# Kernel tuning notes

Hardware: AMD Instinct MI355X
Metric: run time of the kernel (lower is better)

The kernel has to match this reference:

```python
import jax, jax.numpy as jnp
import numpy as np

QC = 13        # quantum_channel
NQ = 12        # qubits per patch circuit
LAYERS12 = 3   # num_layer for FQConv ansatz
LAYERS4 = 4    # layers for the 4-qubit basic ansatz
GROUPS = 10
DIM = 40       # 3*QC + 1 channels
B = 1024
TDIM = 128
EPS = 1e-6     # flax GroupNorm default epsilon
TWO_PI = 2.0 * float(np.pi)


def _take2(s, ax):
    return jnp.take(s, 0, axis=ax), jnp.take(s, 1, axis=ax)


def init_state(n, N):
    # |0...0> state, shape (N, 2, 2, ..., 2); wire w lives on axis w+1
    s = jnp.zeros((N, 2 ** n), jnp.complex64).at[:, 0].set(1.0)
    return s.reshape((N,) + (2,) * n)


def apply_rx(state, theta, w):
    # RX(theta) = [[c, -i s], [-i s, c]], c=cos(theta/2), s=sin(theta/2)
    ax = w + 1
    theta = jnp.asarray(theta, jnp.float32)
    c = jnp.cos(0.5 * theta)
    s = jnp.sin(0.5 * theta)
    if theta.ndim > 0:  # per-sample angles (data embedding)
        sh = (-1,) + (1,) * (state.ndim - 2)
        c = c.reshape(sh)
        s = s.reshape(sh)
    c = c.astype(state.dtype)
    js = (1j * s).astype(state.dtype)
    s0, s1 = _take2(state, ax)
    return jnp.stack([c * s0 - js * s1, c * s1 - js * s0], axis=ax)


def apply_cnot(state, c, t):
    ca = c + 1
    ta = t + 1 if t < c else t  # target axis inside the control=1 slice
    s0, s1 = _take2(state, ca)
    return jnp.stack([s0, jnp.flip(s1, axis=ta)], axis=ca)


def apply_crz(state, theta, c, t):
    # CRZ = diag(1, 1, e^{-i theta/2}, e^{+i theta/2})
    ca = c + 1
    ta = t + 1 if t < c else t
    s0, s1 = _take2(state, ca)
    t0, t1 = _take2(s1, ta)
    em = jnp.exp(-0.5j * theta).astype(state.dtype)
    ep = jnp.exp(0.5j * theta).astype(state.dtype)
    s1 = jnp.stack([em * t0, ep * t1], axis=ta)
    return jnp.stack([s0, s1], axis=ca)


def apply_crx(state, theta, c, t):
    # controlled RX on target when control = 1
    ca = c + 1
    ta = t + 1 if t < c else t
    s0, s1 = _take2(state, ca)
    t0, t1 = _take2(s1, ta)
    ch = jnp.cos(0.5 * theta).astype(state.dtype)
    js = (1j * jnp.sin(0.5 * theta)).astype(state.dtype)
    s1 = jnp.stack([ch * t0 - js * t1, ch * t1 - js * t0], axis=ta)
    return jnp.stack([s0, s1], axis=ca)


def expvals_z(state, n):
    # <Z_w> = P(bit_w = 0) - P(bit_w = 1)
    p = jnp.real(state * jnp.conj(state))
    zs = []
    for w in range(n):
        axes = tuple(a for a in range(1, n + 1) if a != w + 1)
        q = p.sum(axis=axes)  # (N, 2)
        zs.append(q[:, 0] - q[:, 1])
    return jnp.stack(zs, axis=-1)  # (N, n)


def fqconv_layer(state, th):
    # zip(range(11,-1,-4), range(12)) -> i in (11,7,3), j in (0,1,2)
    for j, i in enumerate((11, 7, 3)):
        w1 = [i - 3, i - 2, i - 1, i] + [(i + k) % NQ for k in (1, 2, 3, 4)]
        tj = th[8 * j: 8 * (j + 1)]
        for bi, bj in zip(range(3, -1, -1), range(4)):  # block_C: CRZ
            state = apply_crz(state, TWO_PI * tj[bj], w1[bi + 4], w1[bi])
        for bi, bj in zip(range(3, -1, -1), range(4)):  # block_D: CRX
            state = apply_crx(state, TWO_PI * tj[4 + bj], w1[bi + 4], w1[bi])
    return state


def circuit12(x, theta):
    # x: (N, 12) angles; theta: (72,)
    state = init_state(NQ, x.shape[0])
    for w in range(NQ):  # AngleEmbedding, rotation='X'
        state = apply_rx(state, x[:, w], w)
    for l in range(LAYERS12):
        state = fqconv_layer(state, theta[24 * l: 24 * (l + 1)])
    return expvals_z(state, NQ)


def circuit4(x, theta):
    # Basic_ansatz, 4 qubits, 4 layers, 4 params/layer
    state = init_state(4, x.shape[0])
    for w in range(4):
        state = apply_rx(state, x[:, w], w)
    for l in range(LAYERS4):
        for w in range(4):
            state = apply_rx(state, theta[4 * l + w], w)
        for w in range(3):
            state = apply_cnot(state, w, w + 1)
        state = apply_cnot(state, 3, 0)
    return expvals_z(state, 4)


def run12_all(y, params, circ):
    # scan over the QC per-channel circuits (same structure, different params)
    def body(carry, xp):
        yy, th = xp
        return carry, circ(yy, th)
    _, zs = jax.lax.scan(body, None, (y, params))
    return zs  # (QC, N, 12)


def group_norm(h, scale, bias):
    Bn, H, W, C = h.shape
    g = h.reshape(Bn, H, W, GROUPS, C // GROUPS)
    mu = g.mean(axis=(1, 2, 4), keepdims=True)
    var = g.var(axis=(1, 2, 4), keepdims=True)
    g = (g - mu) * jax.lax.rsqrt(var + EPS)
    return g.reshape(Bn, H, W, C) * scale + bias


def forward(x, time_emb, qparams12, qparams4, gn0_scale, gn0_bias,
            gn1_scale, gn1_bias, time_w, time_b, circ12=circuit12):
    Bn = x.shape[0]

    def qpass(inp, p12_block):
        # per-channel 12-qubit circuits on 2x2x3 patches
        y = jnp.stack([inp[..., 3 * i:3 * (i + 1)].reshape(-1, 12) for i in range(QC)], 0)
        z = run12_all(y, p12_block, circ12)                      # (QC, Bn, 12)
        h1 = jnp.moveaxis(z.reshape(QC, Bn, 2, 2, 3), 0, -2).reshape(Bn, 2, 2, 3 * QC)
        # NOTE: faithful to the source, BOTH passes use circuit/params[-2]
        h4 = circuit4(inp[..., 3 * QC:].reshape(-1, 4), qparams4[0]).reshape(Bn, 2, 2, 1)
        return jnp.concatenate([h1, h4], axis=-1)                 # (Bn, 2, 2, 40)

    h = qpass(x, qparams12[:QC])
    h = group_norm(h, gn0_scale, gn0_bias)
    t = jax.nn.swish(time_emb) @ time_w + time_b                  # (Bn, 2*DIM)
    scale, shift = jnp.split(t[:, None, None, :], 2, axis=-1)
    h = jax.nn.swish(h * (1.0 + scale) + shift)
    h = qpass(h, qparams12[QC:])
    h = jax.nn.swish(group_norm(h, gn1_scale, gn1_bias))
    return x + h  # C == dim, so no res_conv


def setup_inputs() -> dict:
    key = jax.random.key(0)
    ks = jax.random.split(key, 5)
    return {
        "x": jax.random.normal(ks[0], (B, 2, 2, DIM), jnp.float32),
        "time_emb": jax.random.normal(ks[1], (B, TDIM), jnp.float32),
        "qparams12": jax.random.uniform(ks[2], (2 * QC, 24 * LAYERS12), jnp.float32),
        "qparams4": jax.random.uniform(ks[3], (2, 16), jnp.float32),
        "gn0_scale": jnp.ones((DIM,), jnp.float32),
        "gn0_bias": jnp.zeros((DIM,), jnp.float32),
        "gn1_scale": jnp.ones((DIM,), jnp.float32),
        "gn1_bias": jnp.zeros((DIM,), jnp.float32),
        "time_w": jax.random.normal(ks[4], (TDIM, 2 * DIM), jnp.float32) * (TDIM ** -0.5),
        "time_b": jnp.zeros((2 * DIM,), jnp.float32),
    }


def reference(x, time_emb, qparams12, qparams4, gn0_scale, gn0_bias,
              gn1_scale, gn1_bias, time_w, time_b):
    return forward(x, time_emb, qparams12, qparams4, gn0_scale, gn0_bias,
                   gn1_scale, gn1_bias, time_w, time_b)
```

## Files before the change

kernel.cpp:

```cpp
#include <hip/hip_runtime.h>
#include <math.h>


#define PI_F 3.14159265358979323846f

#define DPP_XOR1 0xB1
#define DPP_XOR2 0x4E
#define DPP_XOR8 0x128

typedef float f2 __attribute__((ext_vector_type(2)));

template<int CTRL>
__device__ __forceinline__ float dppf(float x)
{
    return __int_as_float(__builtin_amdgcn_update_dpp(
        __float_as_int(x), __float_as_int(x), CTRL, 0xF, 0xF, false));
}

template<int CTRL>
__device__ __forceinline__ f2 dpp2v(f2 v)
{
    f2 r;
    r[0] = dppf<CTRL>(v[0]);
    r[1] = dppf<CTRL>(v[1]);
    return r;
}

__device__ __forceinline__ float swz4f(float x)
{
    return __int_as_float(__builtin_amdgcn_ds_swizzle(__float_as_int(x), 0x101F));
}

__device__ __forceinline__ f2 swz4v(f2 v)
{
    f2 r;
    r[0] = swz4f(v[0]);
    r[1] = swz4f(v[1]);
    return r;
}

__device__ __forceinline__ float swz16f(float x)
{
    return __int_as_float(__builtin_amdgcn_ds_swizzle(__float_as_int(x), 0x401F));
}

__device__ __forceinline__ f2 swz16v(f2 v)
{
    f2 r;
    r[0] = swz16f(v[0]);
    r[1] = swz16f(v[1]);
    return r;
}

__device__ __forceinline__ float psum16(float x)
{
    float c, d;
    asm("v_mov_b32 %0, %2\n\t"
        "v_mov_b32 %1, %2\n\t"
        "v_permlane16_swap_b32 %0, %1"
        : "=&v"(c), "=&v"(d)
        : "v"(x));
    return c + d;
}

__device__ __forceinline__ float psum32(float x)
{
    float c, d;
    asm("v_mov_b32 %0, %2\n\t"
        "v_mov_b32 %1, %2\n\t"
        "v_permlane32_swap_b32 %0, %1"
        : "=&v"(c), "=&v"(d)
        : "v"(x));
    return c + d;
}

__device__ __forceinline__ void crz_g0_fused(const float* a, f2* R, f2* I,
                                             int lane, int wq)
{
    float gr[4], gi[4];
#pragma unroll
    for (int m = 0; m < 4; ++m) {
        bool cb;
        if      (m == 0) cb = (lane >> 4) & 1;
        else if (m == 1) cb = (lane >> 5) & 1;
        else if (m == 2) cb = wq & 1;
        else             cb = (wq >> 1) & 1;
        gr[m] = cb ? a[2 * m]     : 1.0f;
        gi[m] = cb ? a[2 * m + 1] : 0.0f;
    }
    float u0 = gr[1] * gr[0], v0 = gi[1] * gi[0];
    float w0 = gr[1] * gi[0], z0 = gi[1] * gr[0];
    float p01r[2] = { u0 - v0, u0 + v0 };
    float p01i[2] = { -(w0 + z0), w0 - z0 };
    float u1 = gr[3] * gr[2], v1 = gi[3] * gi[2];
    float w1 = gr[3] * gi[2], z1 = gi[3] * gr[2];
    float p23r[2] = { u1 - v1, u1 + v1 };
    float p23i[2] = { -(w1 + z1), w1 - z1 };

    f2 MrV[4], MiV[4];
#pragma unroll
    for (int p = 0; p < 4; ++p) {
#pragma unroll
        for (int e = 0; e < 2; ++e) {
            const int t = 2 * p + e;
            const int t10 = t & 3, t2 = (t >> 2) & 1;
            float br = (t10 == 0 || t10 == 3) ? p01r[0] : p01r[1];
            float bi = (t10 == 0) ? p01i[0] : (t10 == 1) ? p01i[1]
                     : (t10 == 2) ? -p01i[1] : -p01i[0];
            MrV[p][e] = p23r[t2] * br - p23i[t2] * bi;
            MiV[p][e] = p23r[t2] * bi + p23i[t2] * br;
        }
    }
#pragma unroll
    for (int j = 0; j < 4; ++j) {
        f2 mr = MrV[j], mi = MiV[j];
        f2 r = R[j], im = I[j];
        R[j] = mr * r - mi * im;
        I[j] = mr * im + mi * r;
    }
#pragma unroll
    for (int j = 4; j < 8; ++j) {
        f2 mr = __builtin_shufflevector(MrV[7 - j], MrV[7 - j], 1, 0);
        f2 mi = __builtin_shufflevector(MiV[7 - j], MiV[7 - j], 1, 0);
        f2 r = R[j], im = I[j];
        R[j] = mr * r + mi * im;
        I[j] = mr * im - mi * r;
    }
}

__device__ __forceinline__ void crx_pair(float cg, float sg, f2* R, f2* I)
{
#pragma unroll
    for (int j = 0; j < 8; ++j) {
        f2 r = R[j], im = I[j];
        f2 rs = __builtin_shufflevector(r, r, 1, 0);
        f2 is = __builtin_shufflevector(im, im, 1, 0);
        R[j] = cg * r + sg * is;
        I[j] = cg * im - sg * rs;
    }
}

template<int M>
__device__ __forceinline__ void crx_elem(float cg, float sg, f2* R, f2* I)
{
#pragma unroll
    for (int j = 0; j < 8; ++j) {
        if (j & M) continue;
        const int p = j | M;
        f2 r0 = R[j], i0 = I[j], r1 = R[p], i1 = I[p];
        R[j] = cg * r0 + sg * i1;  I[j] = cg * i0 - sg * r1;
        R[p] = cg * r1 + sg * i0;  I[p] = cg * i1 - sg * r0;
    }
}

__device__ __forceinline__ void crz_e(float cg, float ss, f2* R, f2* I)
{
    const f2 mrv = {1.0f, cg};
    const f2 miv = {0.0f, ss};
#pragma unroll
    for (int j = 0; j < 8; ++j) {
        f2 r = R[j], im = I[j];
        R[j] = mrv * r - miv * im;
        I[j] = mrv * im + miv * r;
    }
}

template<int CB>
__device__ __forceinline__ void crz_ctrlj(float cg, float ss, f2* R, f2* I)
{
#pragma unroll
    for (int j = 0; j < 8; ++j) {
        if (!((j >> CB) & 1)) continue;
        f2 r = R[j], im = I[j];
        R[j] = cg * r - ss * im;
        I[j] = cg * im + ss * r;
    }
}

__device__ __forceinline__ void crx_sh_e(float cg, float sg, f2* R, f2* I)
{
    const f2 cgv = {1.0f, cg};
    const f2 sgv = {0.0f, sg};
#pragma unroll
    for (int j = 0; j < 8; ++j) {
        f2 br = dpp2v<DPP_XOR1>(R[j]);
        f2 bi = dpp2v<DPP_XOR1>(I[j]);
        f2 r = R[j], im = I[j];
        R[j] = cgv * r + sgv * bi;
        I[j] = cgv * im - sgv * br;
    }
}

template<int CB, int CTRL>
__device__ __forceinline__ void crx_shj_dpp(float cg, float sg, f2* R, f2* I)
{
#pragma unroll
    for (int j = 0; j < 8; ++j) {
        if (!((j >> CB) & 1)) continue;
        f2 br = dpp2v<CTRL>(R[j]);
        f2 bi = dpp2v<CTRL>(I[j]);
        f2 r = R[j], im = I[j];
        R[j] = cg * r + sg * bi;
        I[j] = cg * im - sg * br;
    }
}

template<int CB>
__device__ __forceinline__ void crx_shj_swz4(float cg, float sg, f2* R, f2* I)
{
#pragma unroll
    for (int j = 0; j < 8; ++j) {
        if (!((j >> CB) & 1)) continue;
        f2 br = swz4v(R[j]);
        f2 bi = swz4v(I[j]);
        f2 r = R[j], im = I[j];
        R[j] = cg * r + sg * bi;
        I[j] = cg * im - sg * br;
    }
}

__device__ __forceinline__ void crz_g2_fused(const float* a, f2* R, f2* I,
                                             int lane, int wq)
{
    float s0 = ((lane >> 4) & 1) ? a[1] : -a[1];
    bool  c0 = lane & 1;
    float f0r = c0 ? a[0] : 1.0f, f0i = c0 ? s0 : 0.0f;
    float s1 = ((lane >> 5) & 1) ? a[3] : -a[3];
    bool  c1 = (lane >> 1) & 1;
    float f1r = c1 ? a[2] : 1.0f, f1i = c1 ? s1 : 0.0f;
    float s2 = (wq & 1) ? a[5] : -a[5];
    bool  c2 = (lane >> 2) & 1;
    float f2r = c2 ? a[4] : 1.0f, f2i = c2 ? s2 : 0.0f;
    float s3 = ((wq >> 1) & 1) ? a[7] : -a[7];
    bool  c3 = (lane >> 3) & 1;
    float f3r = c3 ? a[6] : 1.0f, f3i = c3 ? s3 : 0.0f;
    float t01r = f0r * f1r - f0i * f1i, t01i = f0r * f1i + f0i * f1r;
    float t23r = f2r * f3r - f2i * f3i, t23i = f2r * f3i + f2i * f3r;
    float Pr = t01r * t23r - t01i * t23i;
    float Pi = t01r * t23i + t01i * t23r;
#pragma unroll
    for (int j = 0; j < 8; ++j) {
        f2 r = R[j], im = I[j];
        R[j] = Pr * r - Pi * im;
        I[j] = Pr * im + Pi * r;
    }
}

__device__ __forceinline__ void crx_swz16_all(float cg, float sg, f2* R, f2* I)
{
#pragma unroll
    for (int j = 0; j < 8; ++j) {
        f2 br = swz16v(R[j]);
        f2 bi = swz16v(I[j]);
        f2 r = R[j], im = I[j];
        R[j] = cg * r + sg * bi;
        I[j] = cg * im - sg * br;
    }
}

__device__ __forceinline__ void crx_perm32(float cg, float sg, f2* R, f2* I)
{
#pragma unroll
    for (int j = 0; j < 8; ++j) {
        float a0 = R[j][0], b0 = I[j][0];
        float a1 = R[j][1], b1 = I[j][1];
        asm("v_permlane32_swap_b32 %0, %1\n\t"
            "v_permlane32_swap_b32 %1, %0" : "+v"(a0), "+v"(b0));
        asm("v_permlane32_swap_b32 %0, %1\n\t"
            "v_permlane32_swap_b32 %1, %0" : "+v"(a1), "+v"(b1));
        f2 A = {a0, a1}, Bv = {b0, b1};
        f2 r = R[j], im = I[j];
        R[j] = cg * r + sg * A;
        I[j] = cg * im - sg * Bv;
    }
}

__global__ void __launch_bounds__(256, 4)
qpass12_kernel(const float* __restrict__ inp, const float* __restrict__ cs,
               float* __restrict__ outp)
{
    __shared__ f2 xbufv[4 * 32 * 17];
    float* xbuff = reinterpret_cast<float*>(xbufv);
    const int ts   = threadIdx.x;
    const int wq   = ts >> 6;
    const int lane = ts & 63;
    const int sim  = blockIdx.x;
    const int ci = sim % 13;
    const int b  = sim / 13;
    const float* csc = cs + ci * 144;
    const int ibase = b * 160 + ci * 3;

    float cw[12], sw[12];
#pragma unroll
    for (int w = 0; w < 12; ++w) {
        float x = inp[ibase + (w / 3) * 40 + (w % 3)];
        __sincosf(0.5f * x, &sw[w], &cw[w]);
    }

    float pref = ((wq >> 1) ? sw[0] : cw[0]) * ((wq & 1) ? sw[1] : cw[1]);
#pragma unroll
    for (int w = 2; w < 8; ++w)
        pref *= ((lane >> (7 - w)) & 1) ? sw[w] : cw[w];

    const int pl = (__popc(lane) + __popc(wq)) & 3;
    float oa = (pl == 0) ? 1.0f : (pl == 2) ? -1.0f : 0.0f;
    float ob = (pl == 1) ? -1.0f : (pl == 3) ? 1.0f : 0.0f;

    f2 R[8], I[8];
#pragma unroll
    for (int j = 0; j < 8; ++j) {
        float base = pref * ((j & 4) ? sw[8] : cw[8]) *
                     ((j & 2) ? sw[9] : cw[9]) * ((j & 1) ? sw[10] : cw[10]);
        f2 v2 = { base * cw[11], base * sw[11] };
        const int q0 = __popc(j) & 3;
        const int q1 = (q0 + 1) & 3;
        const float c0l = (q0 == 0) ? oa : (q0 == 1) ? ob : (q0 == 2) ? -oa : -ob;
        const float c1l = (q0 == 0) ? ob : (q0 == 1) ? -oa : (q0 == 2) ? -ob : oa;
        const float c0h = (q1 == 0) ? oa : (q1 == 1) ? ob : (q1 == 2) ? -oa : -ob;
        const float c1h = (q1 == 0) ? ob : (q1 == 1) ? -oa : (q1 == 2) ? -ob : oa;
        R[j] = f2{ v2[0] * c0l, v2[1] * c0h };
        I[j] = f2{ v2[0] * c1l, v2[1] * c1h };
    }

    const bool act2 = (lane >> 2) & 1;
    const bool act3 = (lane >> 3) & 1;
    const int ai2 = ((lane >> 3) << 2) | (lane & 3);
    const int ai3 = ((lane >> 4) << 3) | (lane & 7);
    f2* xw2 = &xbufv[(wq * 32 + ai2) * 17];
    f2* xr2 = &xbufv[((wq ^ 1) * 32 + ai2) * 17];
    f2* xw3 = &xbufv[(wq * 32 + ai3) * 17];
    f2* xr3 = &xbufv[((wq ^ 2) * 32 + ai3) * 17];

#pragma unroll 1
    for (int l = 0; l < 3; ++l) {
        const float* a = csc + l * 48;

        crz_g0_fused(a, R, I, lane, wq);
        { bool cb = (lane >> 4) & 1;
          crx_pair(cb ? a[ 8] : 1.0f, cb ? a[ 9] : 0.0f, R, I); }
        { bool cb = (lane >> 5) & 1;
          crx_elem<1>(cb ? a[10] : 1.0f, cb ? a[11] : 0.0f, R, I); }
        if (wq & 1)
            crx_elem<2>(a[12], a[13], R, I);
        if ((wq >> 1) & 1)
            crx_elem<4>(a[14], a[15], R, I);

        { float ss = (lane & 1) ? a[17] : -a[17];
          crz_e(a[16], ss, R, I); }
        { float ss = ((lane >> 1) & 1) ? a[19] : -a[19];
          crz_ctrlj<0>(a[18], ss, R, I); }
        { float ss = ((lane >> 2) & 1) ? a[21] : -a[21];
          crz_ctrlj<1>(a[20], ss, R, I); }
        { float ss = ((lane >> 3) & 1) ? a[23] : -a[23];
          crz_ctrlj<2>(a[22], ss, R, I); }
        crx_sh_e(a[24], a[25], R, I);
        crx_shj_dpp<0, DPP_XOR2>(a[26], a[27], R, I);
        crx_shj_swz4<1>(a[28], a[29], R, I);
        crx_shj_dpp<2, DPP_XOR8>(a[30], a[31], R, I);

        crz_g2_fused(a + 32, R, I, lane, wq);
        { bool cb = lane & 1;
          crx_swz16_all(cb ? a[40] : 1.0f, cb ? a[41] : 0.0f, R, I); }
        { bool cb = (lane >> 1) & 1;
          crx_perm32(cb ? a[42] : 1.0f, cb ? a[43] : 0.0f, R, I); }
        __syncthreads();
        if (act2) {
#pragma unroll
            for (int j = 0; j < 8; ++j) {
                xw2[j]     = R[j];
                xw2[8 + j] = I[j];
            }
        }
        __syncthreads();
        if (act2) {
            float cg = a[44], sg = a[45];
#pragma unroll
            for (int j = 0; j < 8; ++j) {
                f2 br = xr2[j], bi = xr2[8 + j];
                f2 r = R[j], im = I[j];
                R[j] = cg * r + sg * bi;
                I[j] = cg * im - sg * br;
            }
        }
        __syncthreads();
        if (act3) {
#pragma unroll
            for (int j = 0; j < 8; ++j) {
                xw3[j]     = R[j];
                xw3[8 + j] = I[j];
            }
        }
        __syncthreads();
        if (act3) {
            float cg = a[46], sg = a[47];
#pragma unroll
            for (int j = 0; j < 8; ++j) {
                f2 br = xr3[j], bi = xr3[8 + j];
                f2 r = R[j], im = I[j];
                R[j] = cg * r + sg * bi;
                I[j] = cg * im - sg * br;
            }
        }
    }

    f2 accT = {0.0f, 0.0f}, acc8 = {0.0f, 0.0f};
    f2 acc9 = {0.0f, 0.0f}, acc10 = {0.0f, 0.0f};
#pragma unroll
    for (int j = 0; j < 8; ++j) {
        f2 p = R[j] * R[j] + I[j] * I[j];
        accT += p;
        if (j & 4) acc8 -= p; else acc8 += p;
        if (j & 2) acc9 -= p; else acc9 += p;
        if (j & 1) acc10 -= p; else acc10 += p;
    }
    float T   = accT[0] + accT[1];
    float A11 = accT[0] - accT[1];
    float A8  = acc8[0] + acc8[1];
    float A9  = acc9[0] + acc9[1];
    float A10 = acc10[0] + acc10[1];

    float dc0, dc1, dc2, dc3, dc4, dc5;
    float x = T;
    { float u = dppf<DPP_XOR1>(x); dc0 = x - u; x += u; }
    { float u = dppf<DPP_XOR2>(x); dc1 = x - u; x += u; }
    { float u = swz4f(x);          dc2 = x - u; x += u; }
    { float u = dppf<DPP_XOR8>(x); dc3 = x - u; x += u; }
    { float s = psum16(x);         dc4 = 2.0f * x - s; x = s; }
    { float s = psum32(x);         dc5 = 2.0f * x - s; x = s; }
    dc0 += dppf<DPP_XOR2>(dc0);
    dc0 += swz4f(dc0);
    dc0 += dppf<DPP_XOR8>(dc0);
    dc0 = psum16(dc0);  dc0 = psum32(dc0);
    dc1 += swz4f(dc1);
    dc1 += dppf<DPP_XOR8>(dc1);
    dc1 = psum16(dc1);  dc1 = psum32(dc1);
    dc2 += dppf<DPP_XOR8>(dc2);
    dc2 = psum16(dc2);  dc2 = psum32(dc2);
    dc3 = psum16(dc3);  dc3 = psum32(dc3);
    dc4 = psum32(dc4);
    A8  += dppf<DPP_XOR1>(A8);   A8  += dppf<DPP_XOR2>(A8);
    A8  += swz4f(A8);            A8  += dppf<DPP_XOR8>(A8);
    A8  = psum16(A8);            A8  = psum32(A8);
    A9  += dppf<DPP_XOR1>(A9);   A9  += dppf<DPP_XOR2>(A9);
    A9  += swz4f(A9);            A9  += dppf<DPP_XOR8>(A9);
    A9  = psum16(A9);            A9  = psum32(A9);
    A10 += dppf<DPP_XOR1>(A10);  A10 += dppf<DPP_XOR2>(A10);
    A10 += swz4f(A10);           A10 += dppf<DPP_XOR8>(A10);
    A10 = psum16(A10);           A10 = psum32(A10);
    A11 += dppf<DPP_XOR1>(A11);  A11 += dppf<DPP_XOR2>(A11);
    A11 += swz4f(A11);           A11 += dppf<DPP_XOR8>(A11);
    A11 = psum16(A11);           A11 = psum32(A11);

    __syncthreads();
    if (lane == 0) {
        float* wv = &xbuff[wq * 12];
        wv[0]  = (wq >> 1) ? -x : x;
        wv[1]  = (wq & 1)  ? -x : x;
        wv[2]  = dc5;
        wv[3]  = dc4;
        wv[4]  = dc3;
        wv[5]  = dc2;
        wv[6]  = dc1;
        wv[7]  = dc0;
        wv[8]  = A8;
        wv[9]  = A9;
        wv[10] = A10;
        wv[11] = A11;
    }
    __syncthreads();
    if (ts < 12) {
        float z = xbuff[ts] + xbuff[12 + ts] + xbuff[24 + ts] + xbuff[36 + ts];
        outp[ibase + (ts / 3) * 40 + (ts % 3)] = z;
    }
}

__global__ void q4_kernel(const float* __restrict__ inp,
                          const float* __restrict__ cs4,
                          float* __restrict__ outp)
{
    int b = blockIdx.x * blockDim.x + threadIdx.x;
    if (b >= 1024) return;
    float cw[4], sw[4];
#pragma unroll
    for (int j = 0; j < 4; ++j) {
        float x = inp[(b * 4 + j) * 40 + 39];
        __sincosf(0.5f * x, &sw[j], &cw[j]);
    }
    float sr[16], si[16];
#pragma unroll
    for (int k = 0; k < 16; ++k) {
        float v = 1.0f;
#pragma unroll
        for (int j = 0; j < 4; ++j)
            v *= ((k >> (3 - j)) & 1) ? sw[j] : cw[j];
        int ph = __popc(k) & 3;
        sr[k] = (ph == 0) ? v : (ph == 2) ? -v : 0.0f;
        si[k] = (ph == 1) ? -v : (ph == 3) ? v : 0.0f;
    }
#pragma unroll
    for (int l = 0; l < 4; ++l) {
#pragma unroll
        for (int w = 0; w < 4; ++w) {
            float cg = cs4[2 * (4 * l + w)], sg = cs4[2 * (4 * l + w) + 1];
            const int m = 1 << (3 - w);
#pragma unroll
            for (int k = 0; k < 16; ++k) {
                if (k & m) continue;
                int p2 = k | m;
                float r0 = sr[k], i0 = si[k], r1 = sr[p2], i1 = si[p2];
                sr[k]  = cg * r0 + sg * i1;  si[k]  = cg * i0 - sg * r1;
                sr[p2] = cg * r1 + sg * i0;  si[p2] = cg * i1 - sg * r0;
            }
        }
#pragma unroll
        for (int e = 0; e < 4; ++e) {
            const int cq = e, tq = (e + 1) & 3;
            const int pcb = 1 << (3 - cq), ptb = 1 << (3 - tq);
#pragma unroll
            for (int k = 0; k < 16; ++k) {
                if (!(k & pcb)) continue;
                if (k & ptb) continue;
                int p2 = k | ptb;
                float tr = sr[k], ti = si[k];
                sr[k] = sr[p2]; si[k] = si[p2];
                sr[p2] = tr;    si[p2] = ti;
            }
        }
    }
    float p[16];
#pragma unroll
    for (int k = 0; k < 16; ++k) p[k] = sr[k] * sr[k] + si[k] * si[k];
#pragma unroll
    for (int j = 0; j < 4; ++j) {
        float z = 0.0f;
#pragma unroll
        for (int k = 0; k < 16; ++k)
            z += ((k >> (3 - j)) & 1) ? -p[k] : p[k];
        outp[(b * 4 + j) * 40 + 39] = z;
    }
}

__global__ void prep_kernel(const float* __restrict__ q12,
                            const float* __restrict__ q4,
                            float* __restrict__ cs12,
                            float* __restrict__ cs4)
{
    int idx = blockIdx.x * 256 + threadIdx.x;
    if (idx < 26 * 72) {
        float s, c;
        sincosf(PI_F * q12[idx], &s, &c);
        cs12[2 * idx]     = c;
        cs12[2 * idx + 1] = s;
    }
    if (idx < 16) {
        float s, c;
        sincosf(0.5f * q4[idx], &s, &c);
        cs4[2 * idx]     = c;
        cs4[2 * idx + 1] = s;
    }
}

__global__ void tmlp_kernel(const float* __restrict__ emb,
                            const float* __restrict__ W,
                            const float* __restrict__ bias,
                            float* __restrict__ t)
{
    __shared__ float se[128];
    int b = blockIdx.x, tid = threadIdx.x;
    float e = emb[b * 128 + tid];
    se[tid] = e / (1.0f + __expf(-e));
    __syncthreads();
    if (tid < 80) {
        float acc = bias[tid];
        for (int k = 0; k < 128; ++k) acc += se[k] * W[k * 80 + tid];
        t[b * 80 + tid] = acc;
    }
}

__global__ void gn0_kernel(const float* __restrict__ h, const float* __restrict__ t,
                           const float* __restrict__ sc, const float* __restrict__ bi,
                           float* __restrict__ outp)
{
    __shared__ float v[160];
    __shared__ float mu[10], rstd[10];
    int b = blockIdx.x, tid = threadIdx.x;
    if (tid < 160) v[tid] = h[b * 160 + tid];
    __syncthreads();
    if (tid < 10) {
        float s1 = 0.0f, s2 = 0.0f;
#pragma unroll
        for (int sp = 0; sp < 4; ++sp)
#pragma unroll
            for (int k = 0; k < 4; ++k) {
                float x = v[sp * 40 + tid * 4 + k];
                s1 += x; s2 += x * x;
            }
        float m = s1 * (1.0f / 16.0f);
        float var = s2 * (1.0f / 16.0f) - m * m;
        mu[tid] = m; rstd[tid] = rsqrtf(var + 1e-6f);
    }
    __syncthreads();
    if (tid < 160) {
        int ch = tid % 40;
        int g = ch >> 2;
        float hn = (v[tid] - mu[g]) * rstd[g] * sc[ch] + bi[ch];
        float scale = t[b * 80 + ch], shift = t[b * 80 + 40 + ch];
        float z = hn * (1.0f + scale) + shift;
        outp[b * 160 + tid] = z / (1.0f + __expf(-z));
    }
}

__global__ void gn1_kernel(const float* __restrict__ h, const float* __restrict__ x,
                           const float* __restrict__ sc, const float* __restrict__ bi,
                           float* __restrict__ outp)
{
    __shared__ float v[160];
    __shared__ float mu[10], rstd[10];
    int b = blockIdx.x, tid = threadIdx.x;
    if (tid < 160) v[tid] = h[b * 160 + tid];
    __syncthreads();
    if (tid < 10) {
        float s1 = 0.0f, s2 = 0.0f;
#pragma unroll
        for (int sp = 0; sp < 4; ++sp)
#pragma unroll
            for (int k = 0; k < 4; ++k) {
                float xx = v[sp * 40 + tid * 4 + k];
                s1 += xx; s2 += xx * xx;
            }
        float m = s1 * (1.0f / 16.0f);
        float var = s2 * (1.0f / 16.0f) - m * m;
        mu[tid] = m; rstd[tid] = rsqrtf(var + 1e-6f);
    }
    __syncthreads();
    if (tid < 160) {
        int ch = tid % 40;
        int g = ch >> 2;
        float hn = (v[tid] - mu[g]) * rstd[g] * sc[ch] + bi[ch];
        float sws = hn / (1.0f + __expf(-hn));
        outp[b * 160 + tid] = x[b * 160 + tid] + sws;
    }
}

extern "C" void kernel_launch(void* const* d_in, const int* in_sizes, int n_in,
                              void* d_out, int out_size, void* d_ws, size_t ws_size,
                              hipStream_t stream)
{
    const float* x    = (const float*)d_in[0];
    const float* temb = (const float*)d_in[1];
    const float* q12  = (const float*)d_in[2];
    const float* q4   = (const float*)d_in[3];
    const float* gn0s = (const float*)d_in[4];
    const float* gn0b = (const float*)d_in[5];
    const float* gn1s = (const float*)d_in[6];
    const float* gn1b = (const float*)d_in[7];
    const float* tw   = (const float*)d_in[8];
    const float* tb   = (const float*)d_in[9];
    float* out = (float*)d_out;

    float* ws   = (float*)d_ws;
    float* cs12 = ws;
    float* cs4  = cs12 + 3744;
    float* tbuf = cs4 + 32;
    float* A    = tbuf + 81920;
    float* Bf   = A + 163840;

    prep_kernel<<<8, 256, 0, stream>>>(q12, q4, cs12, cs4);
    tmlp_kernel<<<1024, 128, 0, stream>>>(temb, tw, tb, tbuf);

    qpass12_kernel<<<13312, 256, 0, stream>>>(x, cs12, A);
    q4_kernel<<<16, 64, 0, stream>>>(x, cs4, A);
    gn0_kernel<<<1024, 160, 0, stream>>>(A, tbuf, gn0s, gn0b, Bf);

    qpass12_kernel<<<13312, 256, 0, stream>>>(Bf, cs12 + 13 * 144, A);
    q4_kernel<<<16, 64, 0, stream>>>(Bf, cs4, A);
    gn1_kernel<<<1024, 160, 0, stream>>>(A, x, gn1s, gn1b, out);
}
```

Before: 540.9 us.

## Fuse two cross-wave CRX exchanges into one LDS round and use bpermute

The two sequential CRX gates that swap amplitudes across waves (via LDS, each with its own pair of barriers) are merged into one exchange. Every lane writes its full state once and reads the three partner waves' states, then applies the combined 2x2 tensor-product rotation in a single step. This removes two barriers and one write/read round per layer, at the cost of a doubled LDS buffer, three reads per element instead of one, and all lanes taking part instead of half. The permlane32 swap is also replaced with ds_bpermute, which moves a cross-half exchange from VALU to the LDS crossbar and may cost latency.

```diff
diff --git a/kernel.cpp b/kernel.cpp
--- a/kernel.cpp
+++ b/kernel.cpp
@@ -258,20 +258,19 @@
     }
 }
 
-__device__ __forceinline__ void crx_perm32(float cg, float sg, f2* R, f2* I)
-{
-#pragma unroll
-    for (int j = 0; j < 8; ++j) {
-        float a0 = R[j][0], b0 = I[j][0];
-        float a1 = R[j][1], b1 = I[j][1];
-        asm("v_permlane32_swap_b32 %0, %1\n\t"
-            "v_permlane32_swap_b32 %1, %0" : "+v"(a0), "+v"(b0));
-        asm("v_permlane32_swap_b32 %0, %1\n\t"
-            "v_permlane32_swap_b32 %1, %0" : "+v"(a1), "+v"(b1));
-        f2 A = {a0, a1}, Bv = {b0, b1};
-        f2 r = R[j], im = I[j];
-        R[j] = cg * r + sg * A;
-        I[j] = cg * im - sg * Bv;
+__device__ __forceinline__ void crx_bperm32(float cg, float sg, f2* R, f2* I,
+                                            int pa)
+{
+#pragma unroll
+    for (int j = 0; j < 8; ++j) {
+        f2 br, bi;
+        br[0] = __int_as_float(__builtin_amdgcn_ds_bpermute(pa, __float_as_int(R[j][0])));
+        br[1] = __int_as_float(__builtin_amdgcn_ds_bpermute(pa, __float_as_int(R[j][1])));
+        bi[0] = __int_as_float(__builtin_amdgcn_ds_bpermute(pa, __float_as_int(I[j][0])));
+        bi[1] = __int_as_float(__builtin_amdgcn_ds_bpermute(pa, __float_as_int(I[j][1])));
+        f2 r = R[j], im = I[j];
+        R[j] = cg * r + sg * bi;
+        I[j] = cg * im - sg * br;
     }
 }
 
@@ -279,7 +278,7 @@
 qpass12_kernel(const float* __restrict__ inp, const float* __restrict__ cs,
                float* __restrict__ outp)
 {
-    __shared__ f2 xbufv[4 * 32 * 17];
+    __shared__ f2 xbufv[4 * 64 * 17];
     float* xbuff = reinterpret_cast<float*>(xbufv);
     const int ts   = threadIdx.x;
     const int wq   = ts >> 6;
@@ -324,12 +323,11 @@
 
     const bool act2 = (lane >> 2) & 1;
     const bool act3 = (lane >> 3) & 1;
-    const int ai2 = ((lane >> 3) << 2) | (lane & 3);
-    const int ai3 = ((lane >> 4) << 3) | (lane & 7);
-    f2* xw2 = &xbufv[(wq * 32 + ai2) * 17];
-    f2* xr2 = &xbufv[((wq ^ 1) * 32 + ai2) * 17];
-    f2* xw3 = &xbufv[(wq * 32 + ai3) * 17];
-    f2* xr3 = &xbufv[((wq ^ 2) * 32 + ai3) * 17];
+    const int  pa   = ((lane ^ 32) << 2);
+    f2* xw = &xbufv[(wq * 64 + lane) * 17];
+    f2* x1 = &xbufv[(((wq ^ 1) * 64) + lane) * 17];
+    f2* x2 = &xbufv[(((wq ^ 2) * 64) + lane) * 17];
+    f2* x3 = &xbufv[(((wq ^ 3) * 64) + lane) * 17];
 
 #pragma unroll 1
     for (int l = 0; l < 3; ++l) {
@@ -362,43 +360,26 @@
         { bool cb = lane & 1;
           crx_swz16_all(cb ? a[40] : 1.0f, cb ? a[41] : 0.0f, R, I); }
         { bool cb = (lane >> 1) & 1;
-          crx_perm32(cb ? a[42] : 1.0f, cb ? a[43] : 0.0f, R, I); }
+          crx_bperm32(cb ? a[42] : 1.0f, cb ? a[43] : 0.0f, R, I, pa); }
         __syncthreads();
-        if (act2) {
-#pragma unroll
-            for (int j = 0; j < 8; ++j) {
-                xw2[j]     = R[j];
-                xw2[8 + j] = I[j];
-            }
+#pragma unroll
+        for (int j = 0; j < 8; ++j) {
+            xw[j]     = R[j];
+            xw[8 + j] = I[j];
         }
         __syncthreads();
-        if (act2) {
-            float cg = a[44], sg = a[45];
+        {
+            float c2 = act2 ? a[44] : 1.0f, s2 = act2 ? a[45] : 0.0f;
+            float c3 = act3 ? a[46] : 1.0f, s3 = act3 ? a[47] : 0.0f;
+            float cc = c2 * c3, sc = s2 * c3, cs = c2 * s3, ss = s2 * s3;
 #pragma unroll
             for (int j = 0; j < 8; ++j) {
-                f2 br = xr2[j], bi = xr2[8 + j];
+                f2 r1 = x1[j], i1 = x1[8 + j];
+                f2 r2 = x2[j], i2 = x2[8 + j];
+                f2 r3 = x3[j], i3 = x3[8 + j];
                 f2 r = R[j], im = I[j];
-                R[j] = cg * r + sg * bi;
-                I[j] = cg * im - sg * br;
-            }
-        }
-        __syncthreads();
-        if (act3) {
-#pragma unroll
-            for (int j = 0; j < 8; ++j) {
-                xw3[j]     = R[j];
-                xw3[8 + j] = I[j];
-            }
-        }
-        __syncthreads();
-        if (act3) {
-            float cg = a[46], sg = a[47];
-#pragma unroll
-            for (int j = 0; j < 8; ++j) {
-                f2 br = xr3[j], bi = xr3[8 + j];
-                f2 r = R[j], im = I[j];
-                R[j] = cg * r + sg * bi;
-                I[j] = cg * im - sg * br;
+                R[j] = cc * r  + sc * i1 + cs * i2 - ss * r3;
+                I[j] = cc * im - sc * r1 - cs * r2 - ss * i3;
             }
         }
     }
```

New measurement: 547.3 us. About the same (+1.2%).
